# Optimization experiments

Measured on AMD Instinct MI355X. Metric: run time of the kernel, lower is better.

## Reference

```python
import jax, jax.numpy as jnp
import numpy as np

NUM_OBJ = 512   # batch_size(8) * objects_per_scene(64)
K = 16          # parts per object
N = NUM_OBJ * K # total part nodes = 8192
P = 512         # points per part
E = NUM_OBJ * K * (K - 1)  # 122880 directed intra-object edges


def setup_inputs() -> dict:
    key = jax.random.key(0)
    ks = jax.random.split(key, 16)

    def w(k, shape, fan_in):
        return jax.random.normal(k, shape, jnp.float32) / np.sqrt(fan_in)

    inp = {}
    inp["pcls_arr"] = jax.random.normal(ks[0], (N, P, 6), jnp.float32)
    # PointNetfeat pointwise convs (6->64->128->256), BN affine params
    inp["W1"] = w(ks[1], (6, 64), 6);     inp["b1"] = jnp.zeros(64);  inp["g1"] = jnp.ones(64);  inp["bt1"] = jnp.zeros(64)
    inp["W2"] = w(ks[2], (64, 128), 64);  inp["b2"] = jnp.zeros(128); inp["g2"] = jnp.ones(128); inp["bt2"] = jnp.zeros(128)
    inp["W3"] = w(ks[3], (128, 256), 128); inp["b3"] = jnp.zeros(256); inp["g3"] = jnp.ones(256); inp["bt3"] = jnp.zeros(256)
    # object_embedding Linear(256->256)
    inp["We"] = w(ks[4], (256, 256), 256); inp["be"] = jnp.zeros(256)
    # two GCN layers (256->256->256)
    inp["Wg1"] = w(ks[5], (256, 256), 256); inp["bg1"] = jnp.zeros(256)
    inp["Wg2"] = w(ks[6], (256, 256), 256); inp["bg2"] = jnp.zeros(256)
    # connectivity head: Linear(512->256), Linear(256->256), Linear(256->1)
    inp["Wc1"] = w(ks[7], (512, 256), 512); inp["bc1"] = jnp.zeros(256)
    inp["Wc2"] = w(ks[8], (256, 256), 256); inp["bc2"] = jnp.zeros(256)
    inp["Wc3"] = w(ks[9], (256, 1), 256);   inp["bc3"] = jnp.zeros(1)
    # dense intra-object directed edges (i != j), matching the nested-loop construction
    ii, jj = np.meshgrid(np.arange(K), np.arange(K), indexing="ij")
    m = ii != jj
    i_loc, j_loc = ii[m], jj[m]            # [K*(K-1)] local pair indices, row-major order
    base = (np.arange(NUM_OBJ) * K)[:, None]
    inp["edge_src"] = jnp.asarray((base + i_loc[None, :]).reshape(-1), jnp.int32)
    inp["edge_dst"] = jnp.asarray((base + j_loc[None, :]).reshape(-1), jnp.int32)
    inp["edge_obj"] = jnp.asarray(np.repeat(np.arange(NUM_OBJ), K * (K - 1)), jnp.int32)
    inp["edge_i"]   = jnp.asarray(np.tile(i_loc, NUM_OBJ), jnp.int32)
    inp["edge_j"]   = jnp.asarray(np.tile(j_loc, NUM_OBJ), jnp.int32)
    return inp


def _bn(x, g, bt):
    # eval-mode BatchNorm with running_mean=0, running_var=1 -> per-channel affine
    return x * g + bt


def _gcn_layer(x, W, b, edge_src, edge_dst):
    # GCNConv with self-loops and symmetric deg^{-1/2} normalization
    xw = x @ W                                               # [N, C]
    deg = jax.ops.segment_sum(jnp.ones(E, x.dtype), edge_dst, num_segments=N) + 1.0
    dinv = deg ** -0.5
    norm = dinv[edge_src] * dinv[edge_dst]                   # [E]
    agg = jax.ops.segment_sum(xw[edge_src] * norm[:, None], edge_dst, num_segments=N)
    agg = agg + xw * (1.0 / deg)[:, None]                    # self-loop term
    return agg + b


def reference(pcls_arr, W1, b1, g1, bt1, W2, b2, g2, bt2, W3, b3, g3, bt3,
              We, be, Wg1, bg1, Wg2, bg2, Wc1, bc1, Wc2, bc2, Wc3, bc3,
              edge_src, edge_dst, edge_obj, edge_i, edge_j):
    # PointNetfeat: pointwise MLP over points, max-pool -> [N, 256]
    h = jax.nn.relu(_bn(pcls_arr @ W1 + b1, g1, bt1))        # [N, P, 64]
    h = jax.nn.relu(_bn(h @ W2 + b2, g2, bt2))               # [N, P, 128]
    h = _bn(h @ W3 + b3, g3, bt3)                            # [N, P, 256]
    feat = jnp.max(h, axis=1)                                # [N, 256]
    emb = feat @ We + be                                     # object_embedding

    # MultiGCN: gcn -> relu -> gcn
    x = jax.nn.relu(_gcn_layer(emb, Wg1, bg1, edge_src, edge_dst))
    x = _gcn_layer(x, Wg2, bg2, edge_src, edge_dst)          # [N, 256]

    # gather parent/child embeddings, concat, connectivity MLP, tanh
    pair = jnp.concatenate([x[edge_src], x[edge_dst]], axis=1)  # [E, 512]
    c = jax.nn.relu(pair @ Wc1 + bc1)
    c = jax.nn.relu(c @ Wc2 + bc2)
    c = jnp.tanh((c @ Wc3 + bc3)[:, 0])                      # [E]

    # scatter edge scores into per-object KxK matrices (zero diagonal)
    out = jnp.zeros((NUM_OBJ, K, K), c.dtype).at[edge_obj, edge_i, edge_j].set(c)
    return out
```

## Files before the change

kernel.cpp:

```cpp
#include <hip/hip_runtime.h>
#include <hip/hip_bf16.h>
#include <stdint.h>
#include <stddef.h>


typedef short bf16x8 __attribute__((ext_vector_type(8)));
typedef short bf16x4 __attribute__((ext_vector_type(4)));
typedef float f32x4  __attribute__((ext_vector_type(4)));

#define WT1_OFF   0u
#define WT2_OFF   4096u
#define WT3_OFF   20480u
#define B1F_OFF   86016u
#define B2F_OFF   86272u
#define B3F_OFF   86784u
#define FSUM_OFF  87808u
#define WC1S_OFF  612096u

__device__ __forceinline__ unsigned short f2bf(float f) {
  union { float f; unsigned u; } v; v.f = f;
  unsigned r = v.u + 0x7fffu + ((v.u >> 16) & 1u);
  return (unsigned short)(r >> 16);
}

__device__ __forceinline__ bf16x4 pack_relu4(f32x4 d) {
  __hip_bfloat162 lo = __float22bfloat162_rn(make_float2(fmaxf(d.x, 0.f), fmaxf(d.y, 0.f)));
  __hip_bfloat162 hi = __float22bfloat162_rn(make_float2(fmaxf(d.z, 0.f), fmaxf(d.w, 0.f)));
  union { bf16x4 v; __hip_bfloat162 h[2]; } u;
  u.h[0] = lo; u.h[1] = hi;
  return u.v;
}

__global__ void prep_kernel(
    const float* __restrict__ W1, const float* __restrict__ b1,
    const float* __restrict__ g1, const float* __restrict__ bt1,
    const float* __restrict__ W2, const float* __restrict__ b2,
    const float* __restrict__ g2, const float* __restrict__ bt2,
    const float* __restrict__ W3, const float* __restrict__ b3,
    const float* __restrict__ g3, const float* __restrict__ bt3,
    const float* __restrict__ Wc1, unsigned char* __restrict__ ws)
{
  unsigned short* wt1 = (unsigned short*)(ws + WT1_OFF);
  unsigned short* wt2 = (unsigned short*)(ws + WT2_OFF);
  unsigned short* wt3 = (unsigned short*)(ws + WT3_OFF);
  float* b1f  = (float*)(ws + B1F_OFF);
  float* b2f  = (float*)(ws + B2F_OFF);
  float* b3f  = (float*)(ws + B3F_OFF);
  float* wc1s = (float*)(ws + WC1S_OFF);

  int i = blockIdx.x * 256 + threadIdx.x;
  if (i < 2048) { int o = i >> 5, c = i & 31;
    float v = (c < 6) ? W1[c*64 + o] * g1[o]
            : (c == 6 ? (b1[o]*g1[o] + bt1[o]) : 0.f);
    wt1[i] = f2bf(v); return; }
  i -= 2048;
  if (i < 8192) { int o = i >> 6, c = i & 63;
    wt2[i] = f2bf(W2[c*128 + o] * g2[o]); return; }
  i -= 8192;
  if (i < 32768) { int o = i >> 7, c = i & 127;
    wt3[i] = f2bf(W3[c*256 + o] * g3[o]); return; }
  i -= 32768;
  if (i < 64)  { b1f[i] = b1[i]*g1[i] + bt1[i]; return; }
  i -= 64;
  if (i < 128) { b2f[i] = b2[i]*g2[i] + bt2[i]; return; }
  i -= 128;
  if (i < 256) { b3f[i] = b3[i]*g3[i] + bt3[i]; return; }
  i -= 256;
  if (i < 65536) { wc1s[i] = Wc1[i] + Wc1[i + 65536]; }
}

#define LDSX  0
#define LDSH1 5120
#define LDSH2 14336

__global__ __launch_bounds__(512)
__attribute__((amdgpu_waves_per_eu(4, 4)))
void pointnet_kernel(
    const float* __restrict__ pcls, const unsigned char* __restrict__ ws,
    float* __restrict__ fsum)
{
  __shared__ __align__(16) unsigned short lds[31744];

  const unsigned short* wt1 = (const unsigned short*)(ws + WT1_OFF);
  const unsigned short* wt2 = (const unsigned short*)(ws + WT2_OFF);
  const unsigned short* wt3 = (const unsigned short*)(ws + WT3_OFF);
  const float* b2f = (const float*)(ws + B2F_OFF);
  const float* b3f = (const float*)(ws + B3F_OFF);

  const int tid  = threadIdx.x;
  const int w    = tid >> 6;
  const int lane = tid & 63;
  const int l15  = lane & 15;
  const int q    = lane >> 4;
  const int obj  = blockIdx.x;

  const int c1t = w & 3;
  const int ph  = w >> 2;

  bf16x8 af1 = *(const bf16x8*)(wt1 + (c1t*16 + l15)*32 + q*8);
  bf16x8 af2[2], af3[2][4];
#pragma unroll
  for (int kf = 0; kf < 2; ++kf)
    af2[kf] = *(const bf16x8*)(wt2 + (w*16 + l15)*64 + kf*32 + q*8);
#pragma unroll
  for (int nt = 0; nt < 2; ++nt)
#pragma unroll
    for (int kf = 0; kf < 4; ++kf)
      af3[nt][kf] = *(const bf16x8*)(wt3 + ((2*w + nt)*16 + l15)*128 + kf*32 + q*8);

  const f32x4 bias2 = *(const f32x4*)(b2f + w*16 + q*4);

  const int i1v = tid < 256;
  int p0 = tid / 6,          c0 = tid - 6*p0;
  int p1 = (512 + tid) / 6,  c1 = (512 + tid) - 6*p1;
  const int soff0 = LDSX + p0*40 + c0;
  const int soff1 = LDSX + p1*40 + c1;

  for (int i = tid; i < 5120; i += 512) lds[i] = 0;
  __syncthreads();
  if (tid < 128) lds[LDSX + tid*40 + 6] = 0x3F80;
  __syncthreads();

  const float* pbase = pcls + (size_t)obj * 49152;
  lds[soff0] = f2bf(pbase[tid]);
  if (i1v) lds[soff1] = f2bf(pbase[512 + tid]);
  __syncthreads();

  f32x4 macc[2];
  float sacc[2][4];
#pragma unroll
  for (int nt = 0; nt < 2; ++nt) {
    macc[nt] = (f32x4){-3e38f, -3e38f, -3e38f, -3e38f};
#pragma unroll
    for (int r = 0; r < 4; ++r) sacc[nt][r] = 0.f;
  }

  for (int cg = 0; cg < 64; ++cg) {
#pragma unroll
    for (int i = 0; i < 4; ++i) {
      const int pt = ph*4 + i;
      bf16x8 b = *(const bf16x8*)(&lds[LDSX + (pt*16 + l15)*40 + q*8]);
      f32x4 d = {0.f, 0.f, 0.f, 0.f};
      d = __builtin_amdgcn_mfma_f32_16x16x32_bf16(af1, b, d, 0, 0, 0);
      *(bf16x4*)(&lds[LDSH1 + (pt*16 + l15)*72 + c1t*16 + q*4]) = pack_relu4(d);
    }
    __syncthreads();

    float pf0, pf1;
    const int havenext = (cg < 63);
    if (havenext) {
      pf0 = pbase[(cg + 1)*768 + tid];
      if (i1v) pf1 = pbase[(cg + 1)*768 + 512 + tid];
    }

#pragma unroll
    for (int pt = 0; pt < 8; ++pt) {
      bf16x8 b0  = *(const bf16x8*)(&lds[LDSH1 + (pt*16 + l15)*72 + q*8]);
      bf16x8 b1v = *(const bf16x8*)(&lds[LDSH1 + (pt*16 + l15)*72 + 32 + q*8]);
      f32x4 d = bias2;
      d = __builtin_amdgcn_mfma_f32_16x16x32_bf16(af2[0], b0,  d, 0, 0, 0);
      d = __builtin_amdgcn_mfma_f32_16x16x32_bf16(af2[1], b1v, d, 0, 0, 0);
      *(bf16x4*)(&lds[LDSH2 + (pt*16 + l15)*136 + w*16 + q*4]) = pack_relu4(d);
    }
    if (havenext) {
      lds[soff0] = f2bf(pf0);
      if (i1v) lds[soff1] = f2bf(pf1);
    }
    __syncthreads();

#pragma unroll
    for (int pt = 0; pt < 8; ++pt) {
      bf16x8 b[4];
#pragma unroll
      for (int kf = 0; kf < 4; ++kf)
        b[kf] = *(const bf16x8*)(&lds[LDSH2 + (pt*16 + l15)*136 + kf*32 + q*8]);
#pragma unroll
      for (int nt = 0; nt < 2; ++nt) {
        f32x4 d = {0.f, 0.f, 0.f, 0.f};
#pragma unroll
        for (int kf = 0; kf < 4; ++kf)
          d = __builtin_amdgcn_mfma_f32_16x16x32_bf16(af3[nt][kf], b[kf], d, 0, 0, 0);
#pragma unroll
        for (int r = 0; r < 4; ++r)
          macc[nt][r] = fmaxf(macc[nt][r], d[r]);
      }
    }
    if ((cg & 3) == 3) {
#pragma unroll
      for (int nt = 0; nt < 2; ++nt) {
#pragma unroll
        for (int r = 0; r < 4; ++r) {
          float v = macc[nt][r];
          v = fmaxf(v, __shfl_xor(v, 1));
          v = fmaxf(v, __shfl_xor(v, 2));
          v = fmaxf(v, __shfl_xor(v, 4));
          v = fmaxf(v, __shfl_xor(v, 8));
          sacc[nt][r] += v;
        }
        macc[nt] = (f32x4){-3e38f, -3e38f, -3e38f, -3e38f};
      }
    }
    __syncthreads();
  }

#pragma unroll
  for (int r = 0; r < 4; ++r) {
    if (l15 == r) {
#pragma unroll
      for (int nt = 0; nt < 2; ++nt) {
        const int ch = (2*w + nt)*16 + q*4 + r;
        fsum[obj*256 + ch] = sacc[nt][r] + 16.f * b3f[ch];
      }
    }
  }
}

__global__ __launch_bounds__(256) void objmlp_kernel(
    const float* __restrict__ We,  const float* __restrict__ be,
    const float* __restrict__ Wg1, const float* __restrict__ bg1,
    const float* __restrict__ Wg2, const float* __restrict__ bg2,
    const float* __restrict__ bc1,
    const float* __restrict__ Wc2, const float* __restrict__ bc2,
    const float* __restrict__ Wc3, const float* __restrict__ bc3,
    const unsigned char* __restrict__ ws, float* __restrict__ out)
{
  const float* fsum = (const float*)(ws + FSUM_OFF);
  const float* Wc1s = (const float*)(ws + WC1S_OFF);
  __shared__ float bufA[4][256], bufB[4][256], red[4][4];
  __shared__ float cval[4];
  const int t = threadIdx.x, ob = blockIdx.x * 4;

#pragma unroll
  for (int o = 0; o < 4; ++o) bufA[o][t] = fsum[(ob + o)*256 + t];
  __syncthreads();

  float acc[4];
#pragma unroll
  for (int o = 0; o < 4; ++o) acc[o] = 0.f;
#pragma unroll 8
  for (int c = 0; c < 256; ++c) {
    float wv = We[c*256 + t];
#pragma unroll
    for (int o = 0; o < 4; ++o) acc[o] += bufA[o][c] * wv;
  }
#pragma unroll
  for (int o = 0; o < 4; ++o) bufB[o][t] = acc[o] + 16.f * be[t];
  __syncthreads();

#pragma unroll
  for (int o = 0; o < 4; ++o) acc[o] = 0.f;
#pragma unroll 8
  for (int c = 0; c < 256; ++c) {
    float wv = Wg1[c*256 + t];
#pragma unroll
    for (int o = 0; o < 4; ++o) acc[o] += bufB[o][c] * wv;
  }
#pragma unroll
  for (int o = 0; o < 4; ++o) bufA[o][t] = fmaxf(acc[o] * 0.0625f + bg1[t], 0.f);
  __syncthreads();

#pragma unroll
  for (int o = 0; o < 4; ++o) acc[o] = 0.f;
#pragma unroll 8
  for (int c = 0; c < 256; ++c) {
    float wv = Wg2[c*256 + t];
#pragma unroll
    for (int o = 0; o < 4; ++o) acc[o] += bufA[o][c] * wv;
  }
#pragma unroll
  for (int o = 0; o < 4; ++o) bufB[o][t] = acc[o] + bg2[t];
  __syncthreads();

#pragma unroll
  for (int o = 0; o < 4; ++o) acc[o] = 0.f;
#pragma unroll 8
  for (int c = 0; c < 256; ++c) {
    float wv = Wc1s[c*256 + t];
#pragma unroll
    for (int o = 0; o < 4; ++o) acc[o] += bufB[o][c] * wv;
  }
#pragma unroll
  for (int o = 0; o < 4; ++o) bufA[o][t] = fmaxf(acc[o] + bc1[t], 0.f);
  __syncthreads();

#pragma unroll
  for (int o = 0; o < 4; ++o) acc[o] = 0.f;
#pragma unroll 8
  for (int c = 0; c < 256; ++c) {
    float wv = Wc2[c*256 + t];
#pragma unroll
    for (int o = 0; o < 4; ++o) acc[o] += bufA[o][c] * wv;
  }

  float w3 = Wc3[t];
#pragma unroll
  for (int o = 0; o < 4; ++o) {
    float part = fmaxf(acc[o] + bc2[t], 0.f) * w3;
#pragma unroll
    for (int off = 1; off < 64; off <<= 1) part += __shfl_xor(part, off);
    if ((t & 63) == 0) red[o][t >> 6] = part;
  }
  __syncthreads();
  if (t < 4) cval[t] = tanhf(red[t][0] + red[t][1] + red[t][2] + red[t][3] + bc3[0]);
  __syncthreads();

  const bool diag = (t >> 4) == (t & 15);
#pragma unroll
  for (int o = 0; o < 4; ++o)
    out[(ob + o)*256 + t] = diag ? 0.f : cval[o];
}

extern "C" void kernel_launch(void* const* d_in, const int* in_sizes, int n_in,
                              void* d_out, int out_size, void* d_ws, size_t ws_size,
                              hipStream_t stream) {
  const float* pcls = (const float*)d_in[0];
  const float* W1 = (const float*)d_in[1];  const float* b1 = (const float*)d_in[2];
  const float* g1 = (const float*)d_in[3];  const float* bt1 = (const float*)d_in[4];
  const float* W2 = (const float*)d_in[5];  const float* b2 = (const float*)d_in[6];
  const float* g2 = (const float*)d_in[7];  const float* bt2 = (const float*)d_in[8];
  const float* W3 = (const float*)d_in[9];  const float* b3 = (const float*)d_in[10];
  const float* g3 = (const float*)d_in[11]; const float* bt3 = (const float*)d_in[12];
  const float* We = (const float*)d_in[13]; const float* be = (const float*)d_in[14];
  const float* Wg1 = (const float*)d_in[15]; const float* bg1 = (const float*)d_in[16];
  const float* Wg2 = (const float*)d_in[17]; const float* bg2 = (const float*)d_in[18];
  const float* Wc1 = (const float*)d_in[19]; const float* bc1 = (const float*)d_in[20];
  const float* Wc2 = (const float*)d_in[21]; const float* bc2 = (const float*)d_in[22];
  const float* Wc3 = (const float*)d_in[23]; const float* bc3 = (const float*)d_in[24];
  unsigned char* ws = (unsigned char*)d_ws;
  float* out = (float*)d_out;

  prep_kernel<<<426, 256, 0, stream>>>(W1, b1, g1, bt1, W2, b2, g2, bt2,
                                       W3, b3, g3, bt3, Wc1, ws);
  pointnet_kernel<<<512, 512, 0, stream>>>(pcls, ws, (float*)(ws + FSUM_OFF));
  objmlp_kernel<<<128, 256, 0, stream>>>(We, be, Wg1, bg1, Wg2, bg2, bc1,
                                         Wc2, bc2, Wc3, bc3, ws, out);
}
```

Measured before the change: 539.3 us.

## Compute layer-1 from registers into double-buffered LDS, removing one barrier per chunk

Each wave now loads its own 16 points directly from global memory into registers, packs them as a bf16 B operand with the bias-one column, and runs all four layer-1 output tiles itself. Results go into one of two ping-pong LDS buffers. The staging of raw points through LDS and one __syncthreads per 128-point chunk go away, and the next chunk's layer 1 overlaps with the current layer 3. In exchange, LDS use and register pressure rise (four A fragments), and only a quarter of the lanes issue the global loads.

```diff
diff --git a/kernel.cpp b/kernel.cpp
--- a/kernel.cpp
+++ b/kernel.cpp
@@ -69,9 +69,8 @@
   if (i < 65536) { wc1s[i] = Wc1[i] + Wc1[i + 65536]; }
 }
 
-#define LDSX  0
-#define LDSH1 5120
-#define LDSH2 14336
+#define LDSH1SZ 9216
+#define LDSH2   18432
 
 __global__ __launch_bounds__(512)
 __attribute__((amdgpu_waves_per_eu(4, 4)))
@@ -79,7 +78,7 @@
     const float* __restrict__ pcls, const unsigned char* __restrict__ ws,
     float* __restrict__ fsum)
 {
-  __shared__ __align__(16) unsigned short lds[31744];
+  __shared__ __align__(16) unsigned short lds[35840];
 
   const unsigned short* wt1 = (const unsigned short*)(ws + WT1_OFF);
   const unsigned short* wt2 = (const unsigned short*)(ws + WT2_OFF);
@@ -94,10 +93,10 @@
   const int q    = lane >> 4;
   const int obj  = blockIdx.x;
 
-  const int c1t = w & 3;
-  const int ph  = w >> 2;
-
-  bf16x8 af1 = *(const bf16x8*)(wt1 + (c1t*16 + l15)*32 + q*8);
+  bf16x8 af1[4];
+#pragma unroll
+  for (int t = 0; t < 4; ++t)
+    af1[t] = *(const bf16x8*)(wt1 + (t*16 + l15)*32 + q*8);
   bf16x8 af2[2], af3[2][4];
 #pragma unroll
   for (int kf = 0; kf < 2; ++kf)
@@ -110,20 +109,35 @@
 
   const f32x4 bias2 = *(const f32x4*)(b2f + w*16 + q*4);
 
-  const int i1v = tid < 256;
-  int p0 = tid / 6,          c0 = tid - 6*p0;
-  int p1 = (512 + tid) / 6,  c1 = (512 + tid) - 6*p1;
-  const int soff0 = LDSX + p0*40 + c0;
-  const int soff1 = LDSX + p1*40 + c1;
-
-  for (int i = tid; i < 5120; i += 512) lds[i] = 0;
-  __syncthreads();
-  if (tid < 128) lds[LDSX + tid*40 + 6] = 0x3F80;
-  __syncthreads();
-
   const float* pbase = pcls + (size_t)obj * 49152;
-  lds[soff0] = f2bf(pbase[tid]);
-  if (i1v) lds[soff1] = f2bf(pbase[512 + tid]);
+  const float* pmine = pbase + (w*16 + l15)*6;
+  const bool  ld = (q == 0);
+
+  {
+    float2 f01, f23, f45;
+    if (ld) {
+      const float* pp = pmine;
+      f01 = *(const float2*)(pp);
+      f23 = *(const float2*)(pp + 2);
+      f45 = *(const float2*)(pp + 4);
+    }
+    bf16x8 bx = (bf16x8){0,0,0,0,0,0,0,0};
+    if (ld) {
+      union { bf16x8 v; __hip_bfloat162 h[4]; } u;
+      u.h[0] = __float22bfloat162_rn(f01);
+      u.h[1] = __float22bfloat162_rn(f23);
+      u.h[2] = __float22bfloat162_rn(f45);
+      u.h[3] = __float22bfloat162_rn(make_float2(1.f, 0.f));
+      bx = u.v;
+    }
+    unsigned short* h1b = &lds[0];
+#pragma unroll
+    for (int t = 0; t < 4; ++t) {
+      f32x4 d = {0.f, 0.f, 0.f, 0.f};
+      d = __builtin_amdgcn_mfma_f32_16x16x32_bf16(af1[t], bx, d, 0, 0, 0);
+      *(bf16x4*)(&h1b[(w*16 + l15)*72 + t*16 + q*4]) = pack_relu4(d);
+    }
+  }
   __syncthreads();
 
   f32x4 macc[2];
@@ -136,37 +150,26 @@
   }
 
   for (int cg = 0; cg < 64; ++cg) {
-#pragma unroll
-    for (int i = 0; i < 4; ++i) {
-      const int pt = ph*4 + i;
-      bf16x8 b = *(const bf16x8*)(&lds[LDSX + (pt*16 + l15)*40 + q*8]);
-      f32x4 d = {0.f, 0.f, 0.f, 0.f};
-      d = __builtin_amdgcn_mfma_f32_16x16x32_bf16(af1, b, d, 0, 0, 0);
-      *(bf16x4*)(&lds[LDSH1 + (pt*16 + l15)*72 + c1t*16 + q*4]) = pack_relu4(d);
-    }
-    __syncthreads();
-
-    float pf0, pf1;
-    const int havenext = (cg < 63);
-    if (havenext) {
-      pf0 = pbase[(cg + 1)*768 + tid];
-      if (i1v) pf1 = pbase[(cg + 1)*768 + 512 + tid];
-    }
-
+    const unsigned short* h1r = &lds[(cg & 1) * LDSH1SZ];
 #pragma unroll
     for (int pt = 0; pt < 8; ++pt) {
-      bf16x8 b0  = *(const bf16x8*)(&lds[LDSH1 + (pt*16 + l15)*72 + q*8]);
-      bf16x8 b1v = *(const bf16x8*)(&lds[LDSH1 + (pt*16 + l15)*72 + 32 + q*8]);
+      bf16x8 b0  = *(const bf16x8*)(&h1r[(pt*16 + l15)*72 + q*8]);
+      bf16x8 b1v = *(const bf16x8*)(&h1r[(pt*16 + l15)*72 + 32 + q*8]);
       f32x4 d = bias2;
       d = __builtin_amdgcn_mfma_f32_16x16x32_bf16(af2[0], b0,  d, 0, 0, 0);
       d = __builtin_amdgcn_mfma_f32_16x16x32_bf16(af2[1], b1v, d, 0, 0, 0);
       *(bf16x4*)(&lds[LDSH2 + (pt*16 + l15)*136 + w*16 + q*4]) = pack_relu4(d);
     }
-    if (havenext) {
-      lds[soff0] = f2bf(pf0);
-      if (i1v) lds[soff1] = f2bf(pf1);
-    }
     __syncthreads();
+
+    const int havenext = (cg < 63);
+    float2 f01, f23, f45;
+    if (havenext && ld) {
+      const float* pp = pmine + (cg + 1)*768;
+      f01 = *(const float2*)(pp);
+      f23 = *(const float2*)(pp + 2);
+      f45 = *(const float2*)(pp + 4);
+    }
 
 #pragma unroll
     for (int pt = 0; pt < 8; ++pt) {
@@ -185,6 +188,26 @@
           macc[nt][r] = fmaxf(macc[nt][r], d[r]);
       }
     }
+
+    if (havenext) {
+      bf16x8 bx = (bf16x8){0,0,0,0,0,0,0,0};
+      if (ld) {
+        union { bf16x8 v; __hip_bfloat162 h[4]; } u;
+        u.h[0] = __float22bfloat162_rn(f01);
+        u.h[1] = __float22bfloat162_rn(f23);
+        u.h[2] = __float22bfloat162_rn(f45);
+        u.h[3] = __float22bfloat162_rn(make_float2(1.f, 0.f));
+        bx = u.v;
+      }
+      unsigned short* h1w = &lds[((cg + 1) & 1) * LDSH1SZ];
+#pragma unroll
+      for (int t = 0; t < 4; ++t) {
+        f32x4 d = {0.f, 0.f, 0.f, 0.f};
+        d = __builtin_amdgcn_mfma_f32_16x16x32_bf16(af1[t], bx, d, 0, 0, 0);
+        *(bf16x4*)(&h1w[(w*16 + l15)*72 + t*16 + q*4]) = pack_relu4(d);
+      }
+    }
+
     if ((cg & 3) == 3) {
 #pragma unroll
       for (int nt = 0; nt < 2; ++nt) {
```

Result: slower. 809.4 us (+50.1%).

## Fuse per-object MLP chain into pointnet kernel epilogue

Applied to the files above, without the earlier changes.

Removes the separate object-MLP kernel and its fsum round trip through global memory. Each pointnet block now runs the five 256x256 matvecs for its own object, with two half-blocks splitting the input channels and combining partials in LDS. The precomputed Wc1 half-sum in prep is dropped, so the fused kernel reads both halves of Wc1 directly. This saves a launch and a global write/read, but each of the 512 blocks now streams all weight matrices alone instead of sharing them across 4 objects per block, which adds L2 traffic and a serial tail to every block.

```diff
diff --git a/kernel.cpp b/kernel.cpp
--- a/kernel.cpp
+++ b/kernel.cpp
@@ -14,8 +14,6 @@
 #define B1F_OFF   86016u
 #define B2F_OFF   86272u
 #define B3F_OFF   86784u
-#define FSUM_OFF  87808u
-#define WC1S_OFF  612096u
 
 __device__ __forceinline__ unsigned short f2bf(float f) {
   union { float f; unsigned u; } v; v.f = f;
@@ -38,7 +36,7 @@
     const float* __restrict__ g2, const float* __restrict__ bt2,
     const float* __restrict__ W3, const float* __restrict__ b3,
     const float* __restrict__ g3, const float* __restrict__ bt3,
-    const float* __restrict__ Wc1, unsigned char* __restrict__ ws)
+    unsigned char* __restrict__ ws)
 {
   unsigned short* wt1 = (unsigned short*)(ws + WT1_OFF);
   unsigned short* wt2 = (unsigned short*)(ws + WT2_OFF);
@@ -46,7 +44,6 @@
   float* b1f  = (float*)(ws + B1F_OFF);
   float* b2f  = (float*)(ws + B2F_OFF);
   float* b3f  = (float*)(ws + B3F_OFF);
-  float* wc1s = (float*)(ws + WC1S_OFF);
 
   int i = blockIdx.x * 256 + threadIdx.x;
   if (i < 2048) { int o = i >> 5, c = i & 31;
@@ -64,9 +61,7 @@
   i -= 64;
   if (i < 128) { b2f[i] = b2[i]*g2[i] + bt2[i]; return; }
   i -= 128;
-  if (i < 256) { b3f[i] = b3[i]*g3[i] + bt3[i]; return; }
-  i -= 256;
-  if (i < 65536) { wc1s[i] = Wc1[i] + Wc1[i + 65536]; }
+  if (i < 256) { b3f[i] = b3[i]*g3[i] + bt3[i]; }
 }
 
 #define LDSX  0
@@ -75,9 +70,15 @@
 
 __global__ __launch_bounds__(512)
 __attribute__((amdgpu_waves_per_eu(4, 4)))
-void pointnet_kernel(
+void pointnet_fused_kernel(
     const float* __restrict__ pcls, const unsigned char* __restrict__ ws,
-    float* __restrict__ fsum)
+    const float* __restrict__ We,  const float* __restrict__ be,
+    const float* __restrict__ Wg1, const float* __restrict__ bg1,
+    const float* __restrict__ Wg2, const float* __restrict__ bg2,
+    const float* __restrict__ Wc1, const float* __restrict__ bc1,
+    const float* __restrict__ Wc2, const float* __restrict__ bc2,
+    const float* __restrict__ Wc3, const float* __restrict__ bc3,
+    float* __restrict__ out)
 {
   __shared__ __align__(16) unsigned short lds[31744];
 
@@ -203,111 +204,83 @@
     __syncthreads();
   }
 
+  float* fls  = (float*)&lds[0];
+  float* fs   = fls;
+  float* bA   = fls + 256;
+  float* bB   = fls + 512;
+  float* part = fls + 768;
+  float* redv = fls + 1280;
+
 #pragma unroll
   for (int r = 0; r < 4; ++r) {
     if (l15 == r) {
 #pragma unroll
       for (int nt = 0; nt < 2; ++nt) {
         const int ch = (2*w + nt)*16 + q*4 + r;
-        fsum[obj*256 + ch] = sacc[nt][r] + 16.f * b3f[ch];
+        fs[ch] = sacc[nt][r] + 16.f * b3f[ch];
       }
     }
   }
-}
-
-__global__ __launch_bounds__(256) void objmlp_kernel(
-    const float* __restrict__ We,  const float* __restrict__ be,
-    const float* __restrict__ Wg1, const float* __restrict__ bg1,
-    const float* __restrict__ Wg2, const float* __restrict__ bg2,
-    const float* __restrict__ bc1,
-    const float* __restrict__ Wc2, const float* __restrict__ bc2,
-    const float* __restrict__ Wc3, const float* __restrict__ bc3,
-    const unsigned char* __restrict__ ws, float* __restrict__ out)
-{
-  const float* fsum = (const float*)(ws + FSUM_OFF);
-  const float* Wc1s = (const float*)(ws + WC1S_OFF);
-  __shared__ float bufA[4][256], bufB[4][256], red[4][4];
-  __shared__ float cval[4];
-  const int t = threadIdx.x, ob = blockIdx.x * 4;
-
-#pragma unroll
-  for (int o = 0; o < 4; ++o) bufA[o][t] = fsum[(ob + o)*256 + t];
-  __syncthreads();
-
-  float acc[4];
-#pragma unroll
-  for (int o = 0; o < 4; ++o) acc[o] = 0.f;
-#pragma unroll 8
-  for (int c = 0; c < 256; ++c) {
-    float wv = We[c*256 + t];
-#pragma unroll
-    for (int o = 0; o < 4; ++o) acc[o] += bufA[o][c] * wv;
+  __syncthreads();
+
+  const int tt = tid & 255, hh = tid >> 8;
+  const int cb = hh * 128;
+  float a;
+
+  a = 0.f;
+#pragma unroll 8
+  for (int c = 0; c < 128; ++c) a += fs[cb + c] * We[(cb + c)*256 + tt];
+  part[hh*256 + tt] = a;
+  __syncthreads();
+  if (hh == 0) bA[tt] = part[tt] + part[256 + tt] + 16.f * be[tt];
+  __syncthreads();
+
+  a = 0.f;
+#pragma unroll 8
+  for (int c = 0; c < 128; ++c) a += bA[cb + c] * Wg1[(cb + c)*256 + tt];
+  part[hh*256 + tt] = a;
+  __syncthreads();
+  if (hh == 0) bB[tt] = fmaxf((part[tt] + part[256 + tt]) * 0.0625f + bg1[tt], 0.f);
+  __syncthreads();
+
+  a = 0.f;
+#pragma unroll 8
+  for (int c = 0; c < 128; ++c) a += bB[cb + c] * Wg2[(cb + c)*256 + tt];
+  part[hh*256 + tt] = a;
+  __syncthreads();
+  if (hh == 0) bA[tt] = part[tt] + part[256 + tt] + bg2[tt];
+  __syncthreads();
+
+  a = 0.f;
+#pragma unroll 8
+  for (int c = 0; c < 128; ++c) {
+    const float xv = bA[cb + c];
+    a += xv * Wc1[(cb + c)*256 + tt];
+    a += xv * Wc1[(cb + c + 256)*256 + tt];
   }
-#pragma unroll
-  for (int o = 0; o < 4; ++o) bufB[o][t] = acc[o] + 16.f * be[t];
-  __syncthreads();
-
-#pragma unroll
-  for (int o = 0; o < 4; ++o) acc[o] = 0.f;
-#pragma unroll 8
-  for (int c = 0; c < 256; ++c) {
-    float wv = Wg1[c*256 + t];
-#pragma unroll
-    for (int o = 0; o < 4; ++o) acc[o] += bufB[o][c] * wv;
-  }
-#pragma unroll
-  for (int o = 0; o < 4; ++o) bufA[o][t] = fmaxf(acc[o] * 0.0625f + bg1[t], 0.f);
-  __syncthreads();
-
-#pragma unroll
-  for (int o = 0; o < 4; ++o) acc[o] = 0.f;
-#pragma unroll 8
-  for (int c = 0; c < 256; ++c) {
-    float wv = Wg2[c*256 + t];
-#pragma unroll
-    for (int o = 0; o < 4; ++o) acc[o] += bufA[o][c] * wv;
-  }
-#pragma unroll
-  for (int o = 0; o < 4; ++o) bufB[o][t] = acc[o] + bg2[t];
-  __syncthreads();
-
-#pragma unroll
-  for (int o = 0; o < 4; ++o) acc[o] = 0.f;
-#pragma unroll 8
-  for (int c = 0; c < 256; ++c) {
-    float wv = Wc1s[c*256 + t];
-#pragma unroll
-    for (int o = 0; o < 4; ++o) acc[o] += bufB[o][c] * wv;
-  }
-#pragma unroll
-  for (int o = 0; o < 4; ++o) bufA[o][t] = fmaxf(acc[o] + bc1[t], 0.f);
-  __syncthreads();
-
-#pragma unroll
-  for (int o = 0; o < 4; ++o) acc[o] = 0.f;
-#pragma unroll 8
-  for (int c = 0; c < 256; ++c) {
-    float wv = Wc2[c*256 + t];
-#pragma unroll
-    for (int o = 0; o < 4; ++o) acc[o] += bufA[o][c] * wv;
-  }
-
-  float w3 = Wc3[t];
-#pragma unroll
-  for (int o = 0; o < 4; ++o) {
-    float part = fmaxf(acc[o] + bc2[t], 0.f) * w3;
-#pragma unroll
-    for (int off = 1; off < 64; off <<= 1) part += __shfl_xor(part, off);
-    if ((t & 63) == 0) red[o][t >> 6] = part;
-  }
-  __syncthreads();
-  if (t < 4) cval[t] = tanhf(red[t][0] + red[t][1] + red[t][2] + red[t][3] + bc3[0]);
-  __syncthreads();
-
-  const bool diag = (t >> 4) == (t & 15);
-#pragma unroll
-  for (int o = 0; o < 4; ++o)
-    out[(ob + o)*256 + t] = diag ? 0.f : cval[o];
+  part[hh*256 + tt] = a;
+  __syncthreads();
+  if (hh == 0) bB[tt] = fmaxf(part[tt] + part[256 + tt] + bc1[tt], 0.f);
+  __syncthreads();
+
+  a = 0.f;
+#pragma unroll 8
+  for (int c = 0; c < 128; ++c) a += bB[cb + c] * Wc2[(cb + c)*256 + tt];
+  part[hh*256 + tt] = a;
+  __syncthreads();
+  if (hh == 0) bA[tt] = fmaxf(part[tt] + part[256 + tt] + bc2[tt], 0.f);
+  __syncthreads();
+
+  float prod = (hh == 0) ? bA[tt] * Wc3[tt] : 0.f;
+#pragma unroll
+  for (int off = 1; off < 64; off <<= 1) prod += __shfl_xor(prod, off);
+  if (lane == 0) redv[w] = prod;
+  __syncthreads();
+  if (tid == 0) redv[0] = tanhf(redv[0] + redv[1] + redv[2] + redv[3] + bc3[0]);
+  __syncthreads();
+  const float cv = redv[0];
+  if (hh == 0)
+    out[obj*256 + tt] = ((tt >> 4) == (tt & 15)) ? 0.f : cv;
 }
 
 extern "C" void kernel_launch(void* const* d_in, const int* in_sizes, int n_in,
@@ -329,9 +302,8 @@
   unsigned char* ws = (unsigned char*)d_ws;
   float* out = (float*)d_out;
 
-  prep_kernel<<<426, 256, 0, stream>>>(W1, b1, g1, bt1, W2, b2, g2, bt2,
-                                       W3, b3, g3, bt3, Wc1, ws);
-  pointnet_kernel<<<512, 512, 0, stream>>>(pcls, ws, (float*)(ws + FSUM_OFF));
-  objmlp_kernel<<<128, 256, 0, stream>>>(We, be, Wg1, bg1, Wg2, bg2, bc1,
-                                         Wc2, bc2, Wc3, bc3, ws, out);
-}
+  prep_kernel<<<170, 256, 0, stream>>>(W1, b1, g1, bt1, W2, b2, g2, bt2,
+                                       W3, b3, g3, bt3, ws);
+  pointnet_fused_kernel<<<512, 512, 0, stream>>>(
+      pcls, ws, We, be, Wg1, bg1, Wg2, bg2, Wc1, bc1, Wc2, bc2, Wc3, bc3, out);
+}
```

Result: faster. 500.7 us (-7.2%).
